# Kernel tuning notes

Measured on AMD Instinct MI355X. Metric: run time of the kernel, lower is better.

The kernel has to match this reference:

```python
import jax, jax.numpy as jnp
import numpy as np

D = 256      # d_model (module-level constant in source)
H = 4        # num_heads
HD = D // H  # head dim = 64
B = 16
T = 512
STEP = 0.5   # self.step_size
NEG = -1e9
SCALE = 1.0 / np.sqrt(HD).astype(np.float32)


def _ln(x, g, b):
    m = jnp.mean(x, -1, keepdims=True)
    v = jnp.var(x, -1, keepdims=True)
    return (x - m) / jnp.sqrt(v + 1e-5) * g + b


def _forward(x, h0,
             sa_wq, sa_wk, sa_wv, sa_wo, sa_bq, sa_bk, sa_bv, sa_bo,
             f_w1, f_b1, f_w2, f_b2,
             ta_wq, ta_wk, ta_wv, ta_wo, ta_bq, ta_bk, ta_bv, ta_bo,
             tr_w1, tr_b1, tr_w2, tr_b2,
             ps_w, ps_b, sp_w, sp_b,
             ln1_g, ln1_b, ln2_g, ln2_b, ln3_g, ln3_b, ln4_g, ln4_b):
    Bz, Tz, Dz = x.shape
    # ---- causal self-attention over parallel_repr ----
    q = (x @ sa_wq + sa_bq).reshape(Bz, Tz, H, HD)
    k = (x @ sa_wk + sa_bk).reshape(Bz, Tz, H, HD)
    v = (x @ sa_wv + sa_bv).reshape(Bz, Tz, H, HD)
    scores = jnp.einsum('bqhd,bkhd->bhqk', q, k) * SCALE
    causal = jnp.tril(jnp.ones((Tz, Tz), bool))
    scores = jnp.where(causal, scores, NEG)
    attn = jnp.einsum('bhqk,bkhd->bqhd', jax.nn.softmax(scores, -1), v)
    attn = attn.reshape(Bz, Tz, Dz) @ sa_wo + sa_bo
    x = _ln(x + attn, ln1_g, ln1_b)
    # ---- FFN with sequential guidance ----
    guid = h0 @ sp_w + sp_b                      # sequential_to_parallel, [B, D]
    ffn_in = x + 0.3 * guid[:, None, :]
    ffn = jax.nn.gelu(ffn_in @ f_w1 + f_b1, approximate=False) @ f_w2 + f_b2
    x = _ln(x + ffn, ln2_g, ln2_b)
    # ---- sequential scan with growing-cache trajectory attention ----
    # past states only enter through their K/V projections, so project each
    # new state once when it is appended (same math as re-projecting the cache).
    def step(carry, inp):
        h, kbuf, vbuf = carry                    # kbuf/vbuf: [T, B, H, HD]
        t, xt = inp                              # xt: [B, D]
        qt = (xt @ ta_wq + ta_bq).reshape(Bz, H, HD)
        sc = jnp.einsum('bhd,tbhd->bht', qt, kbuf) * SCALE
        valid = (jnp.arange(Tz) < t)[None, None, :]
        ctx = jnp.einsum('bht,tbhd->bhd',
                         jax.nn.softmax(jnp.where(valid, sc, NEG), -1), vbuf)
        ctx = ctx.reshape(Bz, Dz) @ ta_wo + ta_bo
        ctx = jnp.where(t > 0, ctx, 0.0)         # torch code zeroes context at t=0
        pg = xt @ ps_w + ps_b                    # parallel_to_sequential
        comb = jnp.concatenate([xt + 0.3 * pg, ctx], -1)
        delta = jax.nn.gelu(comb @ tr_w1 + tr_b1, approximate=False) @ tr_w2 + tr_b2
        h = _ln(h + STEP * delta, ln3_g, ln3_b)
        kbuf = kbuf.at[t].set((h @ ta_wk + ta_bk).reshape(Bz, H, HD))
        vbuf = vbuf.at[t].set((h @ ta_wv + ta_bv).reshape(Bz, H, HD))
        return (h, kbuf, vbuf), None

    buf0 = jnp.zeros((Tz, Bz, H, HD), x.dtype)
    (hT, _, _), _ = jax.lax.scan(step, (h0, buf0, buf0),
                                 (jnp.arange(Tz), jnp.swapaxes(x, 0, 1)))
    return x, _ln(hT, ln4_g, ln4_b)


def setup_inputs() -> dict:
    ks = iter(jax.random.split(jax.random.key(0), 64))
    def w(*shape):
        return jax.random.normal(next(ks), shape, jnp.float32) * 0.02
    inp = {
        'x': jax.random.normal(next(ks), (B, T, D), jnp.float32),
        'h0': jax.random.normal(next(ks), (B, D), jnp.float32),
        'sa_wq': w(D, D), 'sa_wk': w(D, D), 'sa_wv': w(D, D), 'sa_wo': w(D, D),
        'sa_bq': w(D), 'sa_bk': w(D), 'sa_bv': w(D), 'sa_bo': w(D),
        'f_w1': w(D, 4 * D), 'f_b1': w(4 * D), 'f_w2': w(4 * D, D), 'f_b2': w(D),
        'ta_wq': w(D, D), 'ta_wk': w(D, D), 'ta_wv': w(D, D), 'ta_wo': w(D, D),
        'ta_bq': w(D), 'ta_bk': w(D), 'ta_bv': w(D), 'ta_bo': w(D),
        'tr_w1': w(2 * D, 2 * D), 'tr_b1': w(2 * D), 'tr_w2': w(2 * D, D), 'tr_b2': w(D),
        'ps_w': w(D, D), 'ps_b': w(D), 'sp_w': w(D, D), 'sp_b': w(D),
        'ln1_g': jnp.ones(D), 'ln1_b': jnp.zeros(D),
        'ln2_g': jnp.ones(D), 'ln2_b': jnp.zeros(D),
        'ln3_g': jnp.ones(D), 'ln3_b': jnp.zeros(D),
        'ln4_g': jnp.ones(D), 'ln4_b': jnp.zeros(D),
    }
    return inp


def reference(x, h0,
              sa_wq, sa_wk, sa_wv, sa_wo, sa_bq, sa_bk, sa_bv, sa_bo,
              f_w1, f_b1, f_w2, f_b2,
              ta_wq, ta_wk, ta_wv, ta_wo, ta_bq, ta_bk, ta_bv, ta_bo,
              tr_w1, tr_b1, tr_w2, tr_b2,
              ps_w, ps_b, sp_w, sp_b,
              ln1_g, ln1_b, ln2_g, ln2_b, ln3_g, ln3_b, ln4_g, ln4_b):
    return _forward(x, h0,
                    sa_wq, sa_wk, sa_wv, sa_wo, sa_bq, sa_bk, sa_bv, sa_bo,
                    f_w1, f_b1, f_w2, f_b2,
                    ta_wq, ta_wk, ta_wv, ta_wo, ta_bq, ta_bk, ta_bv, ta_bo,
                    tr_w1, tr_b1, tr_w2, tr_b2,
                    ps_w, ps_b, sp_w, sp_b,
                    ln1_g, ln1_b, ln2_g, ln2_b, ln3_g, ln3_b, ln4_g, ln4_b)
```

## Files before the change

kernel.cpp:

```cpp
#include <hip/hip_runtime.h>
#include <hip/hip_bf16.h>

typedef __bf16 bf16x8 __attribute__((ext_vector_type(8)));
typedef float f32x4 __attribute__((ext_vector_type(4)));

__device__ __forceinline__ float b2f(ushort u){
  union { uint u; float f; } x; x.u = ((uint)u) << 16; return x.f;
}
__device__ __forceinline__ ushort f2b(float f){
  union { float f; uint u; } x; x.f = f;
  uint r = x.u + 0x7fff + ((x.u >> 16) & 1);
  return (ushort)(r >> 16);
}
__device__ __forceinline__ uint pack_bf2(float a, float b){
  return (uint)f2b(a) | ((uint)f2b(b) << 16);
}
__device__ __forceinline__ float lo16(uint u){ union{uint a;float f;}x; x.a=u<<16; return x.f; }
__device__ __forceinline__ float hi16(uint u){ union{uint a;float f;}x; x.a=u&0xffff0000u; return x.f; }
__device__ __forceinline__ float gelu_exact(float v){
  return 0.5f * v * (1.0f + erff(v * 0.70710678118654752f));
}

template<int AF32, int ACT>
__global__ __launch_bounds__(256) void gemm_kernel(
    const void* __restrict__ Av, const float* __restrict__ W, int ldw,
    const float* __restrict__ bias, const float* residf,
    float* Cf, ushort* Cb,
    int M, int N, int K, float scale)
{
  __shared__ __align__(16) ushort Al[64*40];
  __shared__ __align__(16) ushort Bl[64*40];
  const int nb = N >> 6;
  const int rb = blockIdx.x / nb, cb = blockIdx.x % nb;
  const int tid = threadIdx.x;
  const int w = tid >> 6, l = tid & 63;
  f32x4 acc[4];
#pragma unroll
  for(int i=0;i<4;i++) acc[i] = (f32x4){0.f,0.f,0.f,0.f};
  const int ar = tid >> 2, ai = (tid & 3) << 3;
  const int bk = tid >> 3, bn = (tid & 7) << 3;
  for(int kb = 0; kb < K; kb += 32){
    uint4 au;
    if(AF32){
      const float* Ap = (const float*)Av + (size_t)(rb*64 + ar)*K + kb + ai;
      float4 f0 = *(const float4*)Ap;
      float4 f1 = *(const float4*)(Ap + 4);
      au.x = pack_bf2(f0.x,f0.y); au.y = pack_bf2(f0.z,f0.w);
      au.z = pack_bf2(f1.x,f1.y); au.w = pack_bf2(f1.z,f1.w);
    } else {
      au = *(const uint4*)((const ushort*)Av + (size_t)(rb*64 + ar)*K + kb + ai);
    }
    const float* Wp = W + (size_t)(kb + bk)*ldw + cb*64 + bn;
    float4 w0 = *(const float4*)Wp;
    float4 w1 = *(const float4*)(Wp + 4);
    ushort bs[8];
    bs[0]=f2b(w0.x); bs[1]=f2b(w0.y); bs[2]=f2b(w0.z); bs[3]=f2b(w0.w);
    bs[4]=f2b(w1.x); bs[5]=f2b(w1.y); bs[6]=f2b(w1.z); bs[7]=f2b(w1.w);
    __syncthreads();
    *(uint4*)&Al[ar*40 + ai] = au;
#pragma unroll
    for(int i=0;i<8;i++) Bl[(bn+i)*40 + bk] = bs[i];
    __syncthreads();
    bf16x8 af = *(const bf16x8*)&Al[(w*16 + (l&15))*40 + (l>>4)*8];
#pragma unroll
    for(int c4=0;c4<4;c4++){
      bf16x8 bfv = *(const bf16x8*)&Bl[(c4*16 + (l&15))*40 + (l>>4)*8];
      acc[c4] = __builtin_amdgcn_mfma_f32_16x16x32_bf16(af, bfv, acc[c4], 0,0,0);
    }
  }
#pragma unroll
  for(int c4=0;c4<4;c4++){
#pragma unroll
    for(int r=0;r<4;r++){
      int row = rb*64 + w*16 + (l>>4)*4 + r;
      int col = cb*64 + c4*16 + (l&15);
      size_t idx = (size_t)row*N + col;
      float vv = acc[c4][r];
      if(bias) vv += bias[col];
      vv *= scale;
      if(residf) vv += residf[idx];
      if(ACT) vv = gelu_exact(vv);
      if(Cf) Cf[idx] = vv;
      if(Cb) Cb[idx] = f2b(vv);
    }
  }
}

__global__ __launch_bounds__(256) void attn_kernel(const ushort* __restrict__ Q,
    const ushort* __restrict__ K, const ushort* __restrict__ V, ushort* __restrict__ O)
{
  __shared__ float s[16*520];
  __shared__ float kt[64*66];
  __shared__ float rowm[16], rowr[16], redx[256];
  const int bid = blockIdx.x;
  const int qb = bid & 31, h = (bid>>5)&3, b = bid>>7;
  const int tid = threadIdx.x;
  const int qi = tid >> 4, jj = tid & 15;
  const int qrow = qb*16 + qi;
  float qreg[64];
  {
    const ushort* qp = Q + ((size_t)(b*512 + qrow))*256 + h*64;
#pragma unroll
    for(int d=0; d<64; d++) qreg[d] = b2f(qp[d])*0.125f;
  }
  const int ntile = (qb*16 + 79) >> 6;
  for(int jt=0; jt<ntile; jt++){
    {
      int jr = tid >> 2, d0 = (tid & 3) << 4;
      const ushort* kp = K + ((size_t)(b*512 + jt*64 + jr))*256 + h*64 + d0;
#pragma unroll
      for(int i=0;i<16;i++) kt[jr*66 + d0 + i] = b2f(kp[i]);
    }
    __syncthreads();
#pragma unroll
    for(int jl=0;jl<4;jl++){
      int jloc = jj*4 + jl;
      int j = jt*64 + jloc;
      float a = 0.f;
#pragma unroll
      for(int d=0; d<64; d++) a += qreg[d]*kt[jloc*66 + d];
      s[qi*520 + j] = (j <= qrow) ? a : -1e30f;
    }
    __syncthreads();
  }
  const int nj = ntile*64;
  float m = -1e30f;
  for(int j=jj; j<nj; j+=16) m = fmaxf(m, s[qi*520 + j]);
  redx[jj*16 + qi] = m;
  __syncthreads();
  if(tid < 16){
    float mm = -1e30f;
#pragma unroll
    for(int k2=0;k2<16;k2++) mm = fmaxf(mm, redx[k2*16 + tid]);
    rowm[tid] = mm;
  }
  __syncthreads();
  float mrow = rowm[qi];
  float ssum = 0.f;
  for(int j=jj; j<nj; j+=16){
    float e = __expf(s[qi*520+j] - mrow);
    s[qi*520+j] = e; ssum += e;
  }
  redx[jj*16 + qi] = ssum;
  __syncthreads();
  if(tid < 16){
    float t2 = 0.f;
#pragma unroll
    for(int k2=0;k2<16;k2++) t2 += redx[k2*16 + tid];
    rowr[tid] = 1.0f/t2;
  }
  const int dd = jj;
  float acc4[4] = {0,0,0,0};
  for(int jt=0; jt<ntile; jt++){
    __syncthreads();
    {
      int jr = tid >> 2, d0 = (tid & 3) << 4;
      const ushort* vp = V + ((size_t)(b*512 + jt*64 + jr))*256 + h*64 + d0;
#pragma unroll
      for(int i=0;i<16;i++) kt[jr*66 + d0 + i] = b2f(vp[i]);
    }
    __syncthreads();
#pragma unroll
    for(int jl=0;jl<64;jl++){
      float p = s[qi*520 + jt*64 + jl];
#pragma unroll
      for(int i=0;i<4;i++) acc4[i] += p*kt[jl*66 + dd*4 + i];
    }
  }
  float rr = rowr[qi];
  ushort* op = O + ((size_t)(b*512 + qrow))*256 + h*64 + dd*4;
#pragma unroll
  for(int i=0;i<4;i++) op[i] = f2b(acc4[i]*rr);
}

__global__ __launch_bounds__(256) void ln_kernel(const float* __restrict__ in,
    const float* __restrict__ g, const float* __restrict__ be,
    float* outf, ushort* outb)
{
  int row = blockIdx.x*4 + (threadIdx.x>>6);
  int lane = threadIdx.x & 63;
  size_t idx = (size_t)row*256 + lane*4;
  float4 v = *(const float4*)(in + idx);
  float s1 = v.x+v.y+v.z+v.w;
  float s2 = v.x*v.x + v.y*v.y + v.z*v.z + v.w*v.w;
#pragma unroll
  for(int off=32; off; off>>=1){ s1 += __shfl_xor(s1,off); s2 += __shfl_xor(s2,off); }
  float mu = s1*(1.f/256.f);
  float var = s2*(1.f/256.f) - mu*mu;
  float r = rsqrtf(var + 1e-5f);
  float vals[4] = {v.x,v.y,v.z,v.w};
  float4 o4; ushort4 ob;
  float* oo = (float*)&o4; ushort* obp = (ushort*)&ob;
#pragma unroll
  for(int i=0;i<4;i++){
    int d = lane*4 + i;
    float y = (vals[i]-mu)*r*g[d] + be[d];
    oo[i] = y; obp[i] = f2b(y);
  }
  if(outf) *(float4*)(outf+idx) = o4;
  if(outb) *(ushort4*)(outb+idx) = ob;
}

__global__ void guid_kernel(const float* __restrict__ h0, const float* __restrict__ spw,
                            const float* __restrict__ spb, float* __restrict__ guid)
{
  int b = blockIdx.x, c = threadIdx.x;
  float s = spb[c];
  for(int r=0;r<256;r++) s += h0[b*256+r]*spw[r*256+c];
  guid[b*256+c] = s;
}

__global__ void ffnin_kernel(const float* __restrict__ x1, const float* __restrict__ guid,
                             ushort* __restrict__ out)
{
  size_t base = ((size_t)blockIdx.x*256 + threadIdx.x)*8;
  int row = (int)(base >> 8); int bb = row >> 9; int c = (int)(base & 255);
  float4 v0 = *(const float4*)(x1 + base);
  float4 v1 = *(const float4*)(x1 + base + 4);
  const float* gp = guid + bb*256 + c;
  const float* xs = (const float*)&v0;
  ushort o[8];
#pragma unroll
  for(int i=0;i<4;i++) o[i] = f2b(xs[i] + 0.3f*gp[i]);
  const float* xs1 = (const float*)&v1;
#pragma unroll
  for(int i=0;i<4;i++) o[4+i] = f2b(xs1[i] + 0.3f*gp[4+i]);
  *(uint4*)(out + base) = *(uint4*)o;
}

__global__ void bo_kernel(const float* __restrict__ ta_bo, const float* __restrict__ tr_w1,
                          float* __restrict__ bo_f)
{
  int c = threadIdx.x;
  float s = 0.f;
  for(int m=0;m<256;m++) s += ta_bo[m]*tr_w1[(size_t)(256+m)*512 + c];
  bo_f[c] = s;
}

__global__ __launch_bounds__(512, 1) void scan_kernel(
    const ushort* __restrict__ qtb, const ushort* __restrict__ Ubf,
    const float* __restrict__ Wf, const float* __restrict__ bo_f,
    float* cbuf, float* dbuf, int* flags,
    const float* __restrict__ ta_wk, const float* __restrict__ ta_wv,
    const float* __restrict__ ta_bk, const float* __restrict__ ta_bv,
    const float* __restrict__ tr_w2, const float* __restrict__ tr_b2,
    const float* __restrict__ ln3_g, const float* __restrict__ ln3_b,
    const float* __restrict__ ln4_g, const float* __restrict__ ln4_b,
    const float* __restrict__ h0, float* __restrict__ out_h)
{
  __shared__ __align__(16) float red[2][1024];
  __shared__ __align__(16) float pbuf[512];
  __shared__ __align__(16) float hbuf[256];
  __shared__ __align__(16) float ctxL[256];
  __shared__ __align__(16) float qbufS[2][64];
  __shared__ float mG[2][16], sG[2][16];
  __shared__ __align__(16) float numS[2][64];
  __shared__ float mzS[2][2];
  __shared__ float sLastP[4];
  __shared__ __align__(16) float glbuf[128];
  __shared__ int cp_same[4];
  extern __shared__ __align__(16) ushort dynL[];
  ushort* kcL = dynL;
  ushort* vcL = dynL + 512*66;

  const int tid = threadIdx.x;
  const int bid = blockIdx.x;
  const int b = bid & 15;
  const int role = bid >> 4;
  const int b4 = b*4;
  const int w8 = tid >> 6;

  if(role < 4){
    for(int i = tid; i < 512*66; i += 512){ kcL[i] = 0; vcL[i] = 0; }
  }

  int myxcc;
  asm volatile("s_getreg_b32 %0, hwreg(HW_REG_XCC_ID)" : "=s"(myxcc));
  if(tid == 0)
    __hip_atomic_store(&flags[256 + bid], myxcc + 1, __ATOMIC_RELEASE, __HIP_MEMORY_SCOPE_AGENT);
  if(tid < 4){
    int cbid = (role < 4) ? (64 + tid*16 + b) : (tid*16 + b);
    int v;
    while((v = __hip_atomic_load(&flags[256 + cbid], __ATOMIC_ACQUIRE, __HIP_MEMORY_SCOPE_AGENT)) == 0)
      __builtin_amdgcn_s_sleep(8);
    cp_same[tid] = ((v - 1) == myxcc);
  }
  __syncthreads();
  const int anyrem = !(cp_same[0] && cp_same[1] && cp_same[2] && cp_same[3]);

  if(role < 4){
    const int hd = role;
    const int bh = b4 + hd;
    const int out = tid >> 2, sX = tid & 3;
    const int kvSel = out >> 6, colX = out & 63;
    const float* WX = kvSel ? ta_wv : ta_wk;
    uint wp[32];
#pragma unroll
    for(int i=0;i<32;i++){
      int r0 = 8*i + 2*sX;
      wp[i] = pack_bf2(WX[(size_t)r0*256 + hd*64 + colX],
                       WX[(size_t)(r0+1)*256 + hd*64 + colX]);
    }
    const float pbX = kvSel ? ta_bv[hd*64 + colX] : ta_bk[hd*64 + colX];
    float h4[4], b2r4[4], g34[4], b34[4];
    if(tid < 64){
#pragma unroll
      for(int c=0;c<4;c++){
        int d = 4*tid + c;
        h4[c] = h0[b*256 + d]; b2r4[c] = tr_b2[d]; g34[c] = ln3_g[d]; b34[c] = ln3_b[d];
      }
      *(float4*)&hbuf[4*tid] = *(float4*)h4;
    }
    const int j_sh = (tid >= 64) ? (tid - 64) : (448 + tid);
    const int gsh = j_sh >> 5;
    const int lsh = tid & 31;
    __syncthreads();

    ushort qpre = 0;
    if(tid >= 448) qpre = qtb[((size_t)(b*512 + 1))*256 + hd*64 + (tid - 448)];

#pragma clang loop unroll(disable)
    for(int t=0;t<512;t++){
      if(tid >= 448){
        qbufS[(t+1)&1][tid-448] = b2f(qpre)*0.125f;
        int tq = (t+2 < 512) ? (t+2) : 511;
        qpre = qtb[((size_t)(b*512 + tq))*256 + hd*64 + (tid - 448)];
      }
      if(t > 0){
        float acc = 0.f;
#pragma unroll
        for(int i=0;i<32;i++){
          float2 hv = *(const float2*)&hbuf[8*i + 2*sX];
          acc += hv.x*lo16(wp[i]) + hv.y*hi16(wp[i]);
        }
        acc += __shfl_xor(acc, 1);
        acc += __shfl_xor(acc, 2);
        float kf = acc + pbX;
        if(sX == 0){
          ushort u = f2b(kf);
          if(kvSel == 0) kcL[(t-1)*66 + colX] = u;
          else           vcL[(t-1)*66 + colX] = u;
        }
        float pv = (kvSel == 0 && sX == 0) ? qbufS[t&1][colX]*kf : 0.f;
        pv += __shfl_xor(pv, 4);
        pv += __shfl_xor(pv, 8);
        pv += __shfl_xor(pv, 16);
        pv += __shfl_xor(pv, 32);
        if(tid < 256 && (tid & 63) == 0) sLastP[tid >> 6] = pv;
        __syncthreads();
        if(tid < 64){
          const int par = t & 1;
          float sl = (sLastP[0] + sLastP[1]) + (sLastP[2] + sLastP[3]);
          float mo = mzS[par][0], Zo = mzS[par][1];
          float m = fmaxf(mo, sl);
          float so = __expf(mo - m);
          float el = __expf(sl - m);
          float Z = Zo*so + el;
          float vlast = b2f(vcL[(t-1)*66 + tid]);
          cbuf[b*256 + hd*64 + tid] = (numS[par][tid]*so + el*vlast) / Z;
          asm volatile("s_waitcnt vmcnt(0)" ::: "memory");
          if(tid == 0){
            *(volatile int*)&flags[bh] = t;
            if(anyrem)
              __hip_atomic_store(&flags[128 + bh], t, __ATOMIC_RELEASE, __HIP_MEMORY_SCOPE_AGENT);
          }
        }
      }

      {
        const int par = (t+1)&1;
        float s = -3.0e38f;
        if(j_sh < t){
          const uint* kr = (const uint*)(kcL + j_sh*66);
          const float* qS = qbufS[par];
          float a = 0.f;
#pragma unroll
          for(int w=0; w<32; w++){
            uint kk = kr[w];
            float2 q2 = *(const float2*)&qS[2*w];
            a += q2.x*lo16(kk) + q2.y*hi16(kk);
          }
          s = a;
        }
        float gm = s;
#pragma unroll
        for(int off=16; off; off>>=1) gm = fmaxf(gm, __shfl_xor(gm, off));
        float e = (j_sh < t) ? __expf(s - gm) : 0.f;
        pbuf[j_sh] = e;
        float gs = e;
#pragma unroll
        for(int off=16; off; off>>=1) gs += __shfl_xor(gs, off);
        if(lsh == 0){ mG[par][gsh] = gm; sG[par][gsh] = gs; }
        int nn = t - gsh*32; nn = nn < 0 ? 0 : (nn > 32 ? 32 : nn);
        float a0 = 0.f, a1 = 0.f;
        const uint* vbase = (const uint*)vcL;
#pragma unroll 4
        for(int i=0;i<nn;i++){
          int j2 = gsh*32 + i;
          uint vv = vbase[j2*33 + lsh];
          float p = pbuf[j2];
          a0 += p*lo16(vv); a1 += p*hi16(vv);
        }
        float2 pr; pr.x = a0; pr.y = a1;
        *(float2*)&red[par][gsh*64 + 2*lsh] = pr;
      }
      __syncthreads();
      if(tid < 64){
        const int par = (t+1)&1;
        float mo = mG[par][0];
#pragma unroll
        for(int g=1; g<16; g++) mo = fmaxf(mo, mG[par][g]);
        float Zo = 0.f, nm = 0.f;
#pragma unroll
        for(int g=0; g<16; g++){
          float scl = __expf(mG[par][g] - mo);
          Zo += sG[par][g]*scl;
          nm += red[par][g*64 + tid]*scl;
        }
        numS[par][tid] = nm;
        if(tid == 0){ mzS[par][0] = mo; mzS[par][1] = Zo; }
      }
      if(tid < 32){
        const int sh = tid >> 3, wv = tid & 7;
        if(cp_same[sh]){
          while(*(volatile int*)&flags[512 + (b4+sh)*8 + wv] < t+1) __builtin_amdgcn_s_sleep(1);
        } else {
          while(__hip_atomic_load(&flags[1024 + (b4+sh)*8 + wv], __ATOMIC_RELAXED, __HIP_MEMORY_SCOPE_AGENT) < t+1)
            __builtin_amdgcn_s_sleep(2);
        }
      }
      if(tid < 64){
        if(anyrem) __builtin_amdgcn_fence(__ATOMIC_ACQUIRE, "agent");
        float ds[4] = {0.f,0.f,0.f,0.f};
#pragma unroll
        for(int i=0;i<4;i++){
          const float* dp = &dbuf[(b4+i)*256 + 4*tid];
#pragma unroll
          for(int c=0;c<4;c++)
            ds[c] += __hip_atomic_load(dp + c, __ATOMIC_RELAXED, __HIP_MEMORY_SCOPE_AGENT);
        }
        float v4[4]; float s1 = 0.f, s2 = 0.f;
#pragma unroll
        for(int c=0;c<4;c++){
          v4[c] = h4[c] + 0.5f*(ds[c] + b2r4[c]);
          s1 += v4[c]; s2 += v4[c]*v4[c];
        }
#pragma unroll
        for(int off=32; off; off>>=1){ s1 += __shfl_xor(s1,off); s2 += __shfl_xor(s2,off); }
        float mu = s1*(1.f/256.f);
        float qq = s2*(1.f/256.f) - mu*mu;
        float rstd = rsqrtf(qq + 1e-5f);
#pragma unroll
        for(int c=0;c<4;c++) h4[c] = (v4[c]-mu)*rstd*g34[c] + b34[c];
        *(float4*)&hbuf[4*tid] = *(float4*)h4;
      }
      __syncthreads();
    }

    if(hd == 0 && tid < 64){
      float s1 = 0.f, s2 = 0.f;
#pragma unroll
      for(int c=0;c<4;c++){ s1 += h4[c]; s2 += h4[c]*h4[c]; }
#pragma unroll
      for(int off=32; off; off>>=1){ s1 += __shfl_xor(s1,off); s2 += __shfl_xor(s2,off); }
      float mu = s1*(1.f/256.f);
      float qq = s2*(1.f/256.f) - mu*mu;
      float rstd = rsqrtf(qq + 1e-5f);
#pragma unroll
      for(int c=0;c<4;c++){
        int d = 4*tid + c;
        out_h[b*256 + d] = (h4[c]-mu)*rstd*ln4_g[d] + ln4_b[d];
      }
    }
  } else {
    const int ish = role - 4;
    const int hid = tid >> 2, sY = tid & 3;
    const int colY = ish*128 + hid;
    uint wfp[32];
#pragma unroll
    for(int i=0;i<32;i++){
      int r0 = 8*i + 2*sY;
      wfp[i] = pack_bf2(Wf[(size_t)r0*512 + colY], Wf[(size_t)(r0+1)*512 + colY]);
    }
    const int dcol = tid >> 1, s2 = tid & 1;
    uint w2p[32];
#pragma unroll
    for(int i=0;i<32;i++){
      int r0 = ish*128 + 4*i + 2*s2;
      w2p[i] = pack_bf2(tr_w2[(size_t)r0*256 + dcol], tr_w2[(size_t)(r0+1)*256 + dcol]);
    }
    const float borr = (sY==0) ? bo_f[colY] : 0.f;
    __syncthreads();

#pragma clang loop unroll(disable)
    for(int t=0;t<512;t++){
      ushort uvs = 0;
      if(sY == 0) uvs = Ubf[((size_t)(b*512 + t))*512 + colY];
      if(t > 0){
        if(tid < 256){
          int q = tid >> 6;
          if(cp_same[q]){
            while(*(volatile int*)&flags[b4 + q] < t) __builtin_amdgcn_s_sleep(1);
          } else {
            while(__hip_atomic_load(&flags[128 + b4 + q], __ATOMIC_RELAXED, __HIP_MEMORY_SCOPE_AGENT) < t)
              __builtin_amdgcn_s_sleep(2);
          }
        }
        if(anyrem) __builtin_amdgcn_fence(__ATOMIC_ACQUIRE, "agent");
        if(tid < 256) ctxL[tid] = *(volatile float*)&cbuf[b*256 + tid];
      }
      __syncthreads();
      float accf = 0.f;
      if(t > 0){
#pragma unroll
        for(int i=0;i<32;i++){
          float2 c2 = *(const float2*)&ctxL[8*i + 2*sY];
          accf += c2.x*lo16(wfp[i]) + c2.y*hi16(wfp[i]);
        }
        accf += __shfl_xor(accf, 1);
        accf += __shfl_xor(accf, 2);
      }
      if(sY == 0){
        float g1 = b2f(uvs) + ((t>0) ? (borr + accf) : 0.f);
        glbuf[hid] = gelu_exact(g1);
      }
      __syncthreads();
      {
        float dp = 0.f;
#pragma unroll
        for(int i=0;i<32;i++){
          float2 gv = *(const float2*)&glbuf[4*i + 2*s2];
          dp += gv.x*lo16(w2p[i]) + gv.y*hi16(w2p[i]);
        }
        dp += __shfl_xor(dp, 1);
        if(s2 == 0) dbuf[(b4+ish)*256 + dcol] = dp;
      }
      asm volatile("s_waitcnt vmcnt(0)" ::: "memory");
      if((tid & 63) == 0){
        *(volatile int*)&flags[512 + (b4+ish)*8 + w8] = t+1;
        if(anyrem)
          __hip_atomic_store(&flags[1024 + (b4+ish)*8 + w8], t+1, __ATOMIC_RELEASE, __HIP_MEMORY_SCOPE_AGENT);
      }
    }
  }
}

#define OFF_FLAGS ((size_t)0)
#define OFF_BOF   ((size_t)8192)
#define OFF_CBUF  ((size_t)16384)
#define OFF_DBUF  ((size_t)32768)
#define OFF_GUID  ((size_t)98304)
#define OFF_WF    ((size_t)131072)
#define OFF_Z1    ((size_t)(1u<<20))
#define OFF_Z2    ((size_t)(5u<<20))
#define OFF_Z3    ((size_t)(9u<<20))
#define OFF_Z4    ((size_t)(13u<<20))
#define OFF_M     ((size_t)(17u<<20))

#define SCAN_DYN_LDS (512*66*2*2)

extern "C" void kernel_launch(void* const* d_in, const int* in_sizes, int n_in,
                              void* d_out, int out_size, void* d_ws, size_t ws_size,
                              hipStream_t stream)
{
  const float* x     = (const float*)d_in[0];
  const float* h0    = (const float*)d_in[1];
  const float* sa_wq = (const float*)d_in[2];
  const float* sa_wk = (const float*)d_in[3];
  const float* sa_wv = (const float*)d_in[4];
  const float* sa_wo = (const float*)d_in[5];
  const float* sa_bq = (const float*)d_in[6];
  const float* sa_bk = (const float*)d_in[7];
  const float* sa_bv = (const float*)d_in[8];
  const float* sa_bo = (const float*)d_in[9];
  const float* f_w1  = (const float*)d_in[10];
  const float* f_b1  = (const float*)d_in[11];
  const float* f_w2  = (const float*)d_in[12];
  const float* f_b2  = (const float*)d_in[13];
  const float* ta_wq = (const float*)d_in[14];
  const float* ta_wk = (const float*)d_in[15];
  const float* ta_wv = (const float*)d_in[16];
  const float* ta_wo = (const float*)d_in[17];
  const float* ta_bq = (const float*)d_in[18];
  const float* ta_bk = (const float*)d_in[19];
  const float* ta_bv = (const float*)d_in[20];
  const float* ta_bo = (const float*)d_in[21];
  const float* tr_w1 = (const float*)d_in[22];
  const float* tr_b1 = (const float*)d_in[23];
  const float* tr_w2 = (const float*)d_in[24];
  const float* tr_b2 = (const float*)d_in[25];
  const float* ps_w  = (const float*)d_in[26];
  const float* ps_b  = (const float*)d_in[27];
  const float* sp_w  = (const float*)d_in[28];
  const float* sp_b  = (const float*)d_in[29];
  const float* ln1_g = (const float*)d_in[30];
  const float* ln1_b = (const float*)d_in[31];
  const float* ln2_g = (const float*)d_in[32];
  const float* ln2_b = (const float*)d_in[33];
  const float* ln3_g = (const float*)d_in[34];
  const float* ln3_b = (const float*)d_in[35];
  const float* ln4_g = (const float*)d_in[36];
  const float* ln4_b = (const float*)d_in[37];

  char* ws = (char*)d_ws;
  int*    flags = (int*)   (ws + OFF_FLAGS);
  float*  bo_f  = (float*) (ws + OFF_BOF);
  float*  cbuf  = (float*) (ws + OFF_CBUF);
  float*  dbuf  = (float*) (ws + OFF_DBUF);
  float*  guid  = (float*) (ws + OFF_GUID);
  float*  Wff   = (float*) (ws + OFF_WF);
  ushort* qb    = (ushort*)(ws + OFF_Z1);
  ushort* kb    = (ushort*)(ws + OFF_Z2);
  ushort* vb    = (ushort*)(ws + OFF_Z3);
  ushort* attnb = (ushort*)(ws + OFF_Z4);
  float*  x0pre = (float*) (ws + OFF_Z1);
  float*  x1f   = (float*) (ws + OFF_Z3);
  ushort* ffnb  = (ushort*)(ws + OFF_M);
  ushort* mid   = (ushort*)(ws + OFF_M + (4u<<20));
  float*  x2pre = (float*) (ws + OFF_Z1);
  ushort* abf   = (ushort*)(ws + OFF_Z4);
  ushort* qtb   = (ushort*)(ws + OFF_Z3);
  ushort* Ubf   = (ushort*)(ws + OFF_M);
  float*  outb  = (float*)d_out;
  float*  out_h = outb + (out_size - 4096);

  static int attr_done = 0;
  if(!attr_done){
    hipFuncSetAttribute((const void*)scan_kernel,
                        hipFuncAttributeMaxDynamicSharedMemorySize, SCAN_DYN_LDS);
    attr_done = 1;
  }

  hipMemsetAsync(flags, 0, 8192, stream);

  gemm_kernel<1,0><<<512, 256, 0, stream>>>(x, sa_wq, 256, sa_bq, nullptr, nullptr, qb, 8192,256,256, 1.0f);
  gemm_kernel<1,0><<<512, 256, 0, stream>>>(x, sa_wk, 256, sa_bk, nullptr, nullptr, kb, 8192,256,256, 1.0f);
  gemm_kernel<1,0><<<512, 256, 0, stream>>>(x, sa_wv, 256, sa_bv, nullptr, nullptr, vb, 8192,256,256, 1.0f);
  attn_kernel<<<2048, 256, 0, stream>>>(qb, kb, vb, attnb);
  gemm_kernel<0,0><<<512, 256, 0, stream>>>(attnb, sa_wo, 256, sa_bo, x, x0pre, nullptr, 8192,256,256, 1.0f);
  ln_kernel<<<2048, 256, 0, stream>>>(x0pre, ln1_g, ln1_b, x1f, nullptr);
  guid_kernel<<<16, 256, 0, stream>>>(h0, sp_w, sp_b, guid);
  ffnin_kernel<<<1024, 256, 0, stream>>>(x1f, guid, ffnb);
  gemm_kernel<0,1><<<1024, 256, 0, stream>>>(ffnb, f_w1, 1024, f_b1, nullptr, nullptr, mid, 8192,512,256, 1.0f);
  gemm_kernel<0,0><<<512, 256, 0, stream>>>(mid, f_w2, 256, f_b2, x1f, x2pre, nullptr, 8192,256,512, 1.0f);
  gemm_kernel<0,1><<<1024, 256, 0, stream>>>(ffnb, f_w1 + 512, 1024, f_b1 + 512, nullptr, nullptr, mid, 8192,512,256, 1.0f);
  gemm_kernel<0,0><<<512, 256, 0, stream>>>(mid, f_w2 + (size_t)512*256, 256, nullptr, x2pre, x2pre, nullptr, 8192,256,512, 1.0f);
  ln_kernel<<<2048, 256, 0, stream>>>(x2pre, ln2_g, ln2_b, outb, nullptr);

  gemm_kernel<1,0><<<512, 256, 0, stream>>>(outb, ps_w, 256, ps_b, outb, nullptr, abf, 8192,256,256, 0.3f);
  gemm_kernel<0,0><<<1024, 256, 0, stream>>>(abf, tr_w1, 512, tr_b1, nullptr, nullptr, Ubf, 8192,512,256, 1.0f);
  gemm_kernel<1,0><<<512, 256, 0, stream>>>(outb, ta_wq, 256, ta_bq, nullptr, nullptr, qtb, 8192,256,256, 1.0f);
  gemm_kernel<1,0><<<32, 256, 0, stream>>>(ta_wo, tr_w1 + (size_t)256*512, 512, nullptr, nullptr, Wff, nullptr, 256,512,256, 1.0f);
  bo_kernel<<<1, 512, 0, stream>>>(ta_bo, tr_w1, bo_f);

  scan_kernel<<<128, 512, SCAN_DYN_LDS, stream>>>(qtb, Ubf, Wff, bo_f, cbuf, dbuf, flags,
                                                  ta_wk, ta_wv, ta_bk, ta_bv, tr_w2, tr_b2,
                                                  ln3_g, ln3_b, ln4_g, ln4_b, h0, out_h);
}
```

Measured before the change: 3.526 ms.

## Batch QKV and PS/TaQ GEMMs, pad attention LDS, split scan dot-product accumulators

Merges the three self-attention projection GEMMs into one launch and the ps/ta_wq projections into another, so fewer kernels are launched and each launch has a larger grid. Changes the attention K/V LDS stride from 66 to 67 to reduce bank conflicts. In the sequential scan kernel, splits the serial dot-product accumulations into four independent partial sums to shorten FMA dependency chains on the per-step critical path. The split accumulators change the floating-point summation order slightly.

Result: slower. 3.692 ms (+4.7%).

```diff
diff --git a/kernel.cpp b/kernel.cpp
--- a/kernel.cpp
+++ b/kernel.cpp
@@ -22,7 +22,7 @@
 }
 
 template<int AF32, int ACT>
-__global__ __launch_bounds__(256) void gemm_kernel(
+__device__ __forceinline__ void gemm_core(int bid,
     const void* __restrict__ Av, const float* __restrict__ W, int ldw,
     const float* __restrict__ bias, const float* residf,
     float* Cf, ushort* Cb,
@@ -31,7 +31,7 @@
   __shared__ __align__(16) ushort Al[64*40];
   __shared__ __align__(16) ushort Bl[64*40];
   const int nb = N >> 6;
-  const int rb = blockIdx.x / nb, cb = blockIdx.x % nb;
+  const int rb = bid / nb, cb = bid % nb;
   const int tid = threadIdx.x;
   const int w = tid >> 6, l = tid & 63;
   f32x4 acc[4];
@@ -86,11 +86,51 @@
   }
 }
 
+template<int AF32, int ACT>
+__global__ __launch_bounds__(256) void gemm_kernel(
+    const void* __restrict__ Av, const float* __restrict__ W, int ldw,
+    const float* __restrict__ bias, const float* residf,
+    float* Cf, ushort* Cb,
+    int M, int N, int K, float scale)
+{
+  gemm_core<AF32,ACT>(blockIdx.x, Av, W, ldw, bias, residf, Cf, Cb, M, N, K, scale);
+}
+
+__global__ __launch_bounds__(256) void gemm_qkv_kernel(
+    const float* __restrict__ x,
+    const float* __restrict__ w0, const float* __restrict__ w1, const float* __restrict__ w2,
+    const float* __restrict__ b0, const float* __restrict__ b1, const float* __restrict__ b2,
+    ushort* c0, ushort* c1, ushort* c2)
+{
+  const int sel = blockIdx.x >> 9;
+  const int bid = blockIdx.x & 511;
+  const float* W = (sel==0) ? w0 : (sel==1) ? w1 : w2;
+  const float* bb = (sel==0) ? b0 : (sel==1) ? b1 : b2;
+  ushort* C = (sel==0) ? c0 : (sel==1) ? c1 : c2;
+  gemm_core<1,0>(bid, x, W, 256, bb, nullptr, nullptr, C, 8192,256,256, 1.0f);
+}
+
+__global__ __launch_bounds__(256) void gemm_pq_kernel(
+    const float* __restrict__ outb,
+    const float* __restrict__ ps_w, const float* __restrict__ ps_b, ushort* abf,
+    const float* __restrict__ ta_wq, const float* __restrict__ ta_bq, ushort* qtb)
+{
+  const int sel = blockIdx.x >> 9;
+  const int bid = blockIdx.x & 511;
+  const float* W = sel ? ta_wq : ps_w;
+  const float* bb = sel ? ta_bq : ps_b;
+  const float* rf = sel ? nullptr : outb;
+  ushort* C = sel ? qtb : abf;
+  float sc = sel ? 1.0f : 0.3f;
+  gemm_core<1,0>(bid, outb, W, 256, bb, rf, nullptr, C, 8192,256,256, sc);
+}
+
+#define KT_S 67
 __global__ __launch_bounds__(256) void attn_kernel(const ushort* __restrict__ Q,
     const ushort* __restrict__ K, const ushort* __restrict__ V, ushort* __restrict__ O)
 {
   __shared__ float s[16*520];
-  __shared__ float kt[64*66];
+  __shared__ float kt[64*KT_S];
   __shared__ float rowm[16], rowr[16], redx[256];
   const int bid = blockIdx.x;
   const int qb = bid & 31, h = (bid>>5)&3, b = bid>>7;
@@ -109,7 +149,7 @@
       int jr = tid >> 2, d0 = (tid & 3) << 4;
       const ushort* kp = K + ((size_t)(b*512 + jt*64 + jr))*256 + h*64 + d0;
 #pragma unroll
-      for(int i=0;i<16;i++) kt[jr*66 + d0 + i] = b2f(kp[i]);
+      for(int i=0;i<16;i++) kt[jr*KT_S + d0 + i] = b2f(kp[i]);
     }
     __syncthreads();
 #pragma unroll
@@ -118,7 +158,7 @@
       int j = jt*64 + jloc;
       float a = 0.f;
 #pragma unroll
-      for(int d=0; d<64; d++) a += qreg[d]*kt[jloc*66 + d];
+      for(int d=0; d<64; d++) a += qreg[d]*kt[jloc*KT_S + d];
       s[qi*520 + j] = (j <= qrow) ? a : -1e30f;
     }
     __syncthreads();
@@ -157,14 +197,14 @@
       int jr = tid >> 2, d0 = (tid & 3) << 4;
       const ushort* vp = V + ((size_t)(b*512 + jt*64 + jr))*256 + h*64 + d0;
 #pragma unroll
-      for(int i=0;i<16;i++) kt[jr*66 + d0 + i] = b2f(vp[i]);
+      for(int i=0;i<16;i++) kt[jr*KT_S + d0 + i] = b2f(vp[i]);
     }
     __syncthreads();
 #pragma unroll
     for(int jl=0;jl<64;jl++){
       float p = s[qi*520 + jt*64 + jl];
 #pragma unroll
-      for(int i=0;i<4;i++) acc4[i] += p*kt[jl*66 + dd*4 + i];
+      for(int i=0;i<4;i++) acc4[i] += p*kt[jl*KT_S + dd*4 + i];
     }
   }
   float rr = rowr[qi];
@@ -327,12 +367,19 @@
         qpre = qtb[((size_t)(b*512 + tq))*256 + hd*64 + (tid - 448)];
       }
       if(t > 0){
-        float acc = 0.f;
-#pragma unroll
-        for(int i=0;i<32;i++){
-          float2 hv = *(const float2*)&hbuf[8*i + 2*sX];
-          acc += hv.x*lo16(wp[i]) + hv.y*hi16(wp[i]);
-        }
+        float aa0=0.f, aa1=0.f, aa2=0.f, aa3=0.f;
+#pragma unroll
+        for(int i=0;i<32;i+=4){
+          float2 h0v = *(const float2*)&hbuf[8*i + 2*sX];
+          float2 h1v = *(const float2*)&hbuf[8*(i+1) + 2*sX];
+          float2 h2v = *(const float2*)&hbuf[8*(i+2) + 2*sX];
+          float2 h3v = *(const float2*)&hbuf[8*(i+3) + 2*sX];
+          aa0 += h0v.x*lo16(wp[i])   + h0v.y*hi16(wp[i]);
+          aa1 += h1v.x*lo16(wp[i+1]) + h1v.y*hi16(wp[i+1]);
+          aa2 += h2v.x*lo16(wp[i+2]) + h2v.y*hi16(wp[i+2]);
+          aa3 += h3v.x*lo16(wp[i+3]) + h3v.y*hi16(wp[i+3]);
+        }
+        float acc = (aa0+aa1)+(aa2+aa3);
         acc += __shfl_xor(acc, 1);
         acc += __shfl_xor(acc, 2);
         float kf = acc + pbX;
@@ -373,14 +420,20 @@
         if(j_sh < t){
           const uint* kr = (const uint*)(kcL + j_sh*66);
           const float* qS = qbufS[par];
-          float a = 0.f;
-#pragma unroll
-          for(int w=0; w<32; w++){
-            uint kk = kr[w];
-            float2 q2 = *(const float2*)&qS[2*w];
-            a += q2.x*lo16(kk) + q2.y*hi16(kk);
+          float a0=0.f, a1=0.f, a2=0.f, a3=0.f;
+#pragma unroll
+          for(int w=0; w<32; w+=4){
+            uint k0 = kr[w], k1 = kr[w+1], k2 = kr[w+2], k3 = kr[w+3];
+            float2 q0 = *(const float2*)&qS[2*w];
+            float2 q1 = *(const float2*)&qS[2*(w+1)];
+            float2 q2 = *(const float2*)&qS[2*(w+2)];
+            float2 q3 = *(const float2*)&qS[2*(w+3)];
+            a0 += q0.x*lo16(k0) + q0.y*hi16(k0);
+            a1 += q1.x*lo16(k1) + q1.y*hi16(k1);
+            a2 += q2.x*lo16(k2) + q2.y*hi16(k2);
+            a3 += q3.x*lo16(k3) + q3.y*hi16(k3);
           }
-          s = a;
+          s = (a0+a1)+(a2+a3);
         }
         float gm = s;
 #pragma unroll
@@ -407,18 +460,21 @@
       __syncthreads();
       if(tid < 64){
         const int par = (t+1)&1;
-        float mo = mG[par][0];
-#pragma unroll
-        for(int g=1; g<16; g++) mo = fmaxf(mo, mG[par][g]);
-        float Zo = 0.f, nm = 0.f;
-#pragma unroll
-        for(int g=0; g<16; g++){
-          float scl = __expf(mG[par][g] - mo);
-          Zo += sG[par][g]*scl;
-          nm += red[par][g*64 + tid]*scl;
-        }
-        numS[par][tid] = nm;
-        if(tid == 0){ mzS[par][0] = mo; mzS[par][1] = Zo; }
+        float m0 = mG[par][0], m1 = mG[par][1];
+#pragma unroll
+        for(int g=2; g<16; g+=2){ m0 = fmaxf(m0, mG[par][g]); m1 = fmaxf(m1, mG[par][g+1]); }
+        float mo = fmaxf(m0, m1);
+        float Zo0=0.f, Zo1=0.f, nm0=0.f, nm1=0.f;
+#pragma unroll
+        for(int g=0; g<16; g+=2){
+          float sc0 = __expf(mG[par][g] - mo);
+          float sc1 = __expf(mG[par][g+1] - mo);
+          Zo0 += sG[par][g]*sc0;   Zo1 += sG[par][g+1]*sc1;
+          nm0 += red[par][g*64 + tid]*sc0;
+          nm1 += red[par][(g+1)*64 + tid]*sc1;
+        }
+        numS[par][tid] = nm0 + nm1;
+        if(tid == 0){ mzS[par][0] = mo; mzS[par][1] = Zo0 + Zo1; }
       }
       if(tid < 32){
         const int sh = tid >> 3, wv = tid & 7;
@@ -512,11 +568,19 @@
       __syncthreads();
       float accf = 0.f;
       if(t > 0){
-#pragma unroll
-        for(int i=0;i<32;i++){
-          float2 c2 = *(const float2*)&ctxL[8*i + 2*sY];
-          accf += c2.x*lo16(wfp[i]) + c2.y*hi16(wfp[i]);
-        }
+        float aa0=0.f, aa1=0.f, aa2=0.f, aa3=0.f;
+#pragma unroll
+        for(int i=0;i<32;i+=4){
+          float2 c0 = *(const float2*)&ctxL[8*i + 2*sY];
+          float2 c1 = *(const float2*)&ctxL[8*(i+1) + 2*sY];
+          float2 c2 = *(const float2*)&ctxL[8*(i+2) + 2*sY];
+          float2 c3 = *(const float2*)&ctxL[8*(i+3) + 2*sY];
+          aa0 += c0.x*lo16(wfp[i])   + c0.y*hi16(wfp[i]);
+          aa1 += c1.x*lo16(wfp[i+1]) + c1.y*hi16(wfp[i+1]);
+          aa2 += c2.x*lo16(wfp[i+2]) + c2.y*hi16(wfp[i+2]);
+          aa3 += c3.x*lo16(wfp[i+3]) + c3.y*hi16(wfp[i+3]);
+        }
+        accf = (aa0+aa1)+(aa2+aa3);
         accf += __shfl_xor(accf, 1);
         accf += __shfl_xor(accf, 2);
       }
@@ -526,12 +590,19 @@
       }
       __syncthreads();
       {
-        float dp = 0.f;
-#pragma unroll
-        for(int i=0;i<32;i++){
-          float2 gv = *(const float2*)&glbuf[4*i + 2*s2];
-          dp += gv.x*lo16(w2p[i]) + gv.y*hi16(w2p[i]);
-        }
+        float aa0=0.f, aa1=0.f, aa2=0.f, aa3=0.f;
+#pragma unroll
+        for(int i=0;i<32;i+=4){
+          float2 g0 = *(const float2*)&glbuf[4*i + 2*s2];
+          float2 g1v = *(const float2*)&glbuf[4*(i+1) + 2*s2];
+          float2 g2 = *(const float2*)&glbuf[4*(i+2) + 2*s2];
+          float2 g3 = *(const float2*)&glbuf[4*(i+3) + 2*s2];
+          aa0 += g0.x*lo16(w2p[i])    + g0.y*hi16(w2p[i]);
+          aa1 += g1v.x*lo16(w2p[i+1]) + g1v.y*hi16(w2p[i+1]);
+          aa2 += g2.x*lo16(w2p[i+2])  + g2.y*hi16(w2p[i+2]);
+          aa3 += g3.x*lo16(w2p[i+3])  + g3.y*hi16(w2p[i+3]);
+        }
+        float dp = (aa0+aa1)+(aa2+aa3);
         dp += __shfl_xor(dp, 1);
         if(s2 == 0) dbuf[(b4+ish)*256 + dcol] = dp;
       }
@@ -633,9 +704,8 @@
 
   hipMemsetAsync(flags, 0, 8192, stream);
 
-  gemm_kernel<1,0><<<512, 256, 0, stream>>>(x, sa_wq, 256, sa_bq, nullptr, nullptr, qb, 8192,256,256, 1.0f);
-  gemm_kernel<1,0><<<512, 256, 0, stream>>>(x, sa_wk, 256, sa_bk, nullptr, nullptr, kb, 8192,256,256, 1.0f);
-  gemm_kernel<1,0><<<512, 256, 0, stream>>>(x, sa_wv, 256, sa_bv, nullptr, nullptr, vb, 8192,256,256, 1.0f);
+  gemm_qkv_kernel<<<1536, 256, 0, stream>>>(x, sa_wq, sa_wk, sa_wv,
+                                            sa_bq, sa_bk, sa_bv, qb, kb, vb);
   attn_kernel<<<2048, 256, 0, stream>>>(qb, kb, vb, attnb);
   gemm_kernel<0,0><<<512, 256, 0, stream>>>(attnb, sa_wo, 256, sa_bo, x, x0pre, nullptr, 8192,256,256, 1.0f);
   ln_kernel<<<2048, 256, 0, stream>>>(x0pre, ln1_g, ln1_b, x1f, nullptr);
@@ -647,9 +717,8 @@
   gemm_kernel<0,0><<<512, 256, 0, stream>>>(mid, f_w2 + (size_t)512*256, 256, nullptr, x2pre, x2pre, nullptr, 8192,256,512, 1.0f);
   ln_kernel<<<2048, 256, 0, stream>>>(x2pre, ln2_g, ln2_b, outb, nullptr);
 
-  gemm_kernel<1,0><<<512, 256, 0, stream>>>(outb, ps_w, 256, ps_b, outb, nullptr, abf, 8192,256,256, 0.3f);
+  gemm_pq_kernel<<<1024, 256, 0, stream>>>(outb, ps_w, ps_b, abf, ta_wq, ta_bq, qtb);
   gemm_kernel<0,0><<<1024, 256, 0, stream>>>(abf, tr_w1, 512, tr_b1, nullptr, nullptr, Ubf, 8192,512,256, 1.0f);
-  gemm_kernel<1,0><<<512, 256, 0, stream>>>(outb, ta_wq, 256, ta_bq, nullptr, nullptr, qtb, 8192,256,256, 1.0f);
   gemm_kernel<1,0><<<32, 256, 0, stream>>>(ta_wo, tr_w1 + (size_t)256*512, 512, nullptr, nullptr, Wff, nullptr, 256,512,256, 1.0f);
   bo_kernel<<<1, 512, 0, stream>>>(ta_bo, tr_w1, bo_f);
 
```
